# Kernel tuning notes

Hardware: AMD Instinct MI355X
Metric: run time of the kernel (lower is better)

Reference implementation:

```python
import jax, jax.numpy as jnp
import numpy as np

CE_W, TRI_W, CEN_W, ALN_W, BAL_W = 1.0, 1.0, 0.0005, 0.5, 0.1
LS_EPS = 0.1      # label smoothing
MARGIN = 0.3      # triplet margin
F_ALPHA, F_GAMMA = 0.25, 2.0


def setup_inputs() -> dict:
    key = jax.random.key(0)
    ks = jax.random.split(key, 7)
    B, C, D = 1024, 8000, 2048
    return {
        "logits": jax.random.normal(ks[0], (B, C), jnp.float32),
        "features": jax.random.normal(ks[1], (B, D), jnp.float32),
        "feat_rgb": jax.random.normal(ks[2], (B, D), jnp.float32),
        "feat_ir": jax.random.normal(ks[3], (B, D), jnp.float32),
        "modality_weights": jax.random.uniform(ks[4], (B, 2), jnp.float32),
        "centers": jax.random.uniform(ks[5], (C, D), jnp.float32, -1.0, 1.0),
        "labels": jax.random.randint(ks[6], (B,), 0, 64),
    }


def reference(logits, features, feat_rgb, feat_ir, modality_weights, centers, labels):
    B, C = logits.shape
    logp = jax.nn.log_softmax(logits, axis=-1)                      # [B, C]
    logp_y = jnp.take_along_axis(logp, labels[:, None], axis=1)[:, 0]
    # CrossEntropy with label smoothing 0.1 (torch semantics)
    ce = jnp.mean(-(1.0 - LS_EPS) * logp_y - LS_EPS * jnp.mean(logp, axis=-1))
    # Focal loss (faithful to source: uses logpt, so term is <= 0)
    ce_ns = -logp_y
    pt = jnp.exp(-ce_ns)
    focal = jnp.mean(F_ALPHA * (1.0 - pt) ** F_GAMMA * (-ce_ns))
    # Batch-hard triplet (vectorized replacement for per-row python loop)
    sq = jnp.sum(features ** 2, axis=1)
    d2 = jnp.maximum(sq[:, None] + sq[None, :] - 2.0 * (features @ features.T), 0.0)
    dist = jnp.where(d2 > 0, jnp.sqrt(jnp.where(d2 > 0, d2, 1.0)), 0.0)  # safe sqrt
    eq = labels[:, None] == labels[None, :]
    eye = jnp.eye(B, dtype=bool)
    pos_mask = eq & ~eye
    neg_mask = ~eq
    hp = jnp.max(jnp.where(pos_mask, dist, -1.0), axis=1)   # hardest positive
    hn = jnp.min(jnp.where(neg_mask, dist, 1e9), axis=1)    # hardest negative
    valid = jnp.any(pos_mask, axis=1) & jnp.any(neg_mask, axis=1)
    tl = jax.nn.relu(hp - hn + MARGIN)
    triplet = jnp.sum(jnp.where(valid, tl, 0.0)) / jnp.maximum(jnp.sum(valid), 1)
    # Center loss (centers gathered and detached)
    cen = jnp.mean((features - jax.lax.stop_gradient(centers[labels])) ** 2)
    # Modality alignment (single rgb-ir pair): mean(1 - cos)
    f1 = feat_rgb / jnp.maximum(jnp.linalg.norm(feat_rgb, axis=1, keepdims=True), 1e-12)
    f2 = feat_ir / jnp.maximum(jnp.linalg.norm(feat_ir, axis=1, keepdims=True), 1e-12)
    align = jnp.mean(1.0 - jnp.sum(f1 * f2, axis=1))
    # Modality balance: max_entropy - entropy
    ent = jnp.mean(-jnp.sum(modality_weights * jnp.log(modality_weights + 1e-8), axis=1))
    balance = jnp.log(jnp.float32(modality_weights.shape[1])) - ent
    # Modality consistency: mse to detached mean over modalities
    mean_feat = jax.lax.stop_gradient(0.5 * (feat_rgb + feat_ir))
    cons = 0.5 * (jnp.mean((feat_rgb - mean_feat) ** 2) + jnp.mean((feat_ir - mean_feat) ** 2))
    total = (CE_W * (0.7 * ce + 0.3 * focal) + TRI_W * triplet + CEN_W * cen
             + ALN_W * align + BAL_W * balance + 0.1 * cons)
    return jnp.stack([total, ce, focal, triplet, cen, align, balance, cons])
```

## Files before the change

kernel.cpp:

```cpp
#include <hip/hip_runtime.h>
#include <math.h>

#define NB 1024
#define NC 8000
#define ND 2048
#define FBS 2080

#define WS_SQ   0
#define WS_CE   1024
#define WS_FO   2048
#define WS_CEN  3072
#define WS_AL   4096
#define WS_CO   5120
#define WS_HPM  6144
#define WS_HNM  22528
#define WS_FB_BYTES 262144

#define NTILES 136
#define NT     32

typedef __attribute__((ext_vector_type(8))) short bf16x8;
typedef __attribute__((ext_vector_type(4))) float f32x4;
#define GLOB __attribute__((address_space(1)))
#define LDSP __attribute__((address_space(3)))

__device__ inline unsigned short f2bf(float f) {
    unsigned u = __float_as_uint(f);
    u += 0x7FFFu + ((u >> 16) & 1u);
    return (unsigned short)(u >> 16);
}

__global__ __launch_bounds__(256) void k_feat(const float* __restrict__ F,
                                              const float* __restrict__ RGB,
                                              const float* __restrict__ IR,
                                              const float* __restrict__ CEN,
                                              const int* __restrict__ labels,
                                              float* __restrict__ ws,
                                              unsigned short* __restrict__ Fb) {
    const int tid = threadIdx.x;
    const int lane = tid & 63, wid = tid >> 6;
    const int row = blockIdx.x * 4 + wid;
    const float4* f4 = (const float4*)(F + (size_t)row * ND);
    const float4* c4 = (const float4*)(CEN + (size_t)labels[row] * ND);
    const float4* r4 = (const float4*)(RGB + (size_t)row * ND);
    const float4* g4 = (const float4*)(IR + (size_t)row * ND);
    ushort4* fb4 = (ushort4*)(Fb + (size_t)row * FBS);

    float s_ff = 0, s_fc = 0, s_rr = 0, s_ii = 0, s_ri = 0, s_dd = 0;
#pragma unroll 4
    for (int t = 0; t < (ND / 4) / 64; ++t) {
        const int q = t * 64 + lane;
        float4 f = f4[q], c = c4[q], r = r4[q], g = g4[q];
        ushort4 h;
        h.x = f2bf(f.x); h.y = f2bf(f.y); h.z = f2bf(f.z); h.w = f2bf(f.w);
        fb4[q] = h;
        float fa[4] = {f.x, f.y, f.z, f.w};
        float ca[4] = {c.x, c.y, c.z, c.w};
        float ra[4] = {r.x, r.y, r.z, r.w};
        float ga[4] = {g.x, g.y, g.z, g.w};
#pragma unroll
        for (int k = 0; k < 4; ++k) {
            s_ff = fmaf(fa[k], fa[k], s_ff);
            float d = fa[k] - ca[k];
            s_fc = fmaf(d, d, s_fc);
            s_rr = fmaf(ra[k], ra[k], s_rr);
            s_ii = fmaf(ga[k], ga[k], s_ii);
            s_ri = fmaf(ra[k], ga[k], s_ri);
            float e = ra[k] - ga[k];
            s_dd = fmaf(e, e, s_dd);
        }
    }
#pragma unroll
    for (int off = 32; off > 0; off >>= 1) {
        s_ff += __shfl_down(s_ff, off);
        s_fc += __shfl_down(s_fc, off);
        s_rr += __shfl_down(s_rr, off);
        s_ii += __shfl_down(s_ii, off);
        s_ri += __shfl_down(s_ri, off);
        s_dd += __shfl_down(s_dd, off);
    }
    if (lane == 0) {
        ws[WS_SQ + row] = s_ff;
        ws[WS_CEN + row] = s_fc;
        float nr = fmaxf(sqrtf(s_rr), 1e-12f);
        float ni = fmaxf(sqrtf(s_ii), 1e-12f);
        ws[WS_AL + row] = 1.0f - s_ri / (nr * ni);
        ws[WS_CO + row] = s_dd;
    }
}

__global__ __launch_bounds__(256) void k_main(const unsigned short* __restrict__ Fb,
                                              const float* __restrict__ logits,
                                              const int* __restrict__ labels,
                                              float* __restrict__ ws) {
    __shared__ __align__(16) unsigned short As[2][64 * 64];
    __shared__ __align__(16) unsigned short Bs[2][64 * 64];
    __shared__ int lr[64], lc[64];
    __shared__ float sqr[64], sqc[64];
    __shared__ float hplR[64], hnlR[64], hplC[64], hnlC[64];
    __shared__ float rs[4], rsx[4];

    const int tid = threadIdx.x;
    const int lane = tid & 63, wid = tid >> 6;

    if (blockIdx.x < NTILES) {
        int rem = blockIdx.x, rp = 0;
        while (rem >= 16 - rp) { rem -= 16 - rp; rp++; }
        const int cp = rp + rem;
        const int row0 = rp << 6, col0 = cp << 6;
        const float* sq = ws + WS_SQ;

        if (tid < 64) {
            lr[tid] = labels[row0 + tid];
            sqr[tid] = sq[row0 + tid];
            hplR[tid] = -1.0f;
            hnlR[tid] = 1e9f;
        } else if (tid < 128) {
            int t = tid - 64;
            lc[t] = labels[col0 + t];
            sqc[t] = sq[col0 + t];
            hplC[t] = -1.0f;
            hnlC[t] = 1e9f;
        }

        const int r8 = lane >> 3;
        const int sl = lane & 7;
        const int soEl = ((sl ^ r8) * 8);

#define STAGE(IT, BUF) do {                                                              \
    const int k0_ = (IT) * 64;                                                           \
    _Pragma("unroll")                                                                    \
    for (int t = 0; t < 2; ++t) {                                                        \
        const int rb_ = wid * 16 + t * 8;                                                \
        __builtin_amdgcn_global_load_lds(                                                \
            (const GLOB unsigned int*)(Fb + (size_t)(row0 + rb_ + r8) * FBS + k0_ + soEl),\
            (LDSP unsigned int*)&As[BUF][rb_ * 64], 16, 0, 0);                           \
        __builtin_amdgcn_global_load_lds(                                                \
            (const GLOB unsigned int*)(Fb + (size_t)(col0 + rb_ + r8) * FBS + k0_ + soEl),\
            (LDSP unsigned int*)&Bs[BUF][rb_ * 64], 16, 0, 0);                           \
    }                                                                                    \
} while (0)

        const int wr = wid >> 1, wc = wid & 1;
        f32x4 acc[2][2] = {};

        STAGE(0, 0);
        int cur = 0;
#pragma unroll 1
        for (int it = 0; it < NT; ++it) {
            if (it + 1 < NT) {
                STAGE(it + 1, cur ^ 1);
                asm volatile("s_waitcnt vmcnt(4)" ::: "memory");
            } else {
                asm volatile("s_waitcnt vmcnt(0)" ::: "memory");
            }
            __builtin_amdgcn_sched_barrier(0);
            __builtin_amdgcn_s_barrier();

            const char* Ab = (const char*)&As[cur][0];
            const char* Bb = (const char*)&Bs[cur][0];
#pragma unroll
            for (int kk = 0; kk < 2; ++kk) {
                const int kb = kk * 64 + (lane >> 4) * 16;
                const int xo = (lane & 7) << 4;
                bf16x8 a[2], b[2];
#pragma unroll
                for (int mi = 0; mi < 2; ++mi) {
                    const int rt = wr * 32 + mi * 16 + (lane & 15);
                    a[mi] = *(const bf16x8*)(Ab + rt * 128 + (kb ^ xo));
                }
#pragma unroll
                for (int ni = 0; ni < 2; ++ni) {
                    const int ct = wc * 32 + ni * 16 + (lane & 15);
                    b[ni] = *(const bf16x8*)(Bb + ct * 128 + (kb ^ xo));
                }
#pragma unroll
                for (int mi = 0; mi < 2; ++mi)
#pragma unroll
                    for (int ni = 0; ni < 2; ++ni)
                        acc[mi][ni] = __builtin_amdgcn_mfma_f32_16x16x32_bf16(a[mi], b[ni], acc[mi][ni], 0, 0, 0);
            }

            __builtin_amdgcn_sched_barrier(0);
            __builtin_amdgcn_s_barrier();
            cur ^= 1;
        }
#undef STAGE

#pragma unroll
        for (int mi = 0; mi < 2; ++mi) {
#pragma unroll
            for (int reg = 0; reg < 4; ++reg) {
                const int rt = wr * 32 + mi * 16 + (lane >> 4) * 4 + reg;
                const int lbr = lr[rt];
                const float sr = sqr[rt];
                float myhp = -1.0f, myhn = 1e9f;
#pragma unroll
                for (int ni = 0; ni < 2; ++ni) {
                    const int ct = wc * 32 + ni * 16 + (lane & 15);
                    float d2 = sr + sqc[ct] - 2.0f * acc[mi][ni][reg];
                    float dist = sqrtf(fmaxf(d2, 0.0f));
                    if (row0 + rt != col0 + ct) {
                        if (lbr == lc[ct]) myhp = fmaxf(myhp, dist);
                        else               myhn = fminf(myhn, dist);
                    }
                }
#pragma unroll
                for (int off = 1; off < 16; off <<= 1) {
                    myhp = fmaxf(myhp, __shfl_xor(myhp, off, 16));
                    myhn = fminf(myhn, __shfl_xor(myhn, off, 16));
                }
                if ((lane & 15) == 0) {
                    atomicMax((int*)&hplR[rt], __float_as_int(myhp));
                    atomicMin((int*)&hnlR[rt], __float_as_int(myhn));
                }
            }
        }

        if (rp != cp) {
#pragma unroll
            for (int ni = 0; ni < 2; ++ni) {
                const int ct = wc * 32 + ni * 16 + (lane & 15);
                const int lbc = lc[ct];
                const float sc = sqc[ct];
                float myhp = -1.0f, myhn = 1e9f;
#pragma unroll
                for (int mi = 0; mi < 2; ++mi) {
#pragma unroll
                    for (int reg = 0; reg < 4; ++reg) {
                        const int rt = wr * 32 + mi * 16 + (lane >> 4) * 4 + reg;
                        float d2 = sqr[rt] + sc - 2.0f * acc[mi][ni][reg];
                        float dist = sqrtf(fmaxf(d2, 0.0f));
                        if (lr[rt] == lbc) myhp = fmaxf(myhp, dist);
                        else               myhn = fminf(myhn, dist);
                    }
                }
                myhp = fmaxf(myhp, __shfl_xor(myhp, 16));
                myhn = fminf(myhn, __shfl_xor(myhn, 16));
                myhp = fmaxf(myhp, __shfl_xor(myhp, 32));
                myhn = fminf(myhn, __shfl_xor(myhn, 32));
                if ((lane >> 4) == 0) {
                    atomicMax((int*)&hplC[ct], __float_as_int(myhp));
                    atomicMin((int*)&hnlC[ct], __float_as_int(myhn));
                }
            }
        }
        __syncthreads();
        if (tid < 64) {
            ws[WS_HPM + (size_t)(row0 + tid) * 16 + cp] = hplR[tid];
            ws[WS_HNM + (size_t)(row0 + tid) * 16 + cp] = hnlR[tid];
        } else if (tid < 128 && rp != cp) {
            int t = tid - 64;
            ws[WS_HPM + (size_t)(col0 + t) * 16 + rp] = hplC[t];
            ws[WS_HNM + (size_t)(col0 + t) * 16 + rp] = hnlC[t];
        }
    } else {
        const int row = blockIdx.x - NTILES;
        const float* x = logits + (size_t)row * NC;
        const float4* x4 = (const float4*)x;
        float xl = 0.0f;
        if (tid == 0) xl = x[labels[row]];

        float s = 0.0f, sx = 0.0f;
        for (int q = tid; q < NC / 4; q += 256) {
            float4 v = x4[q];
            float vv[4] = {v.x, v.y, v.z, v.w};
#pragma unroll
            for (int c = 0; c < 4; ++c) {
                sx += vv[c];
                s += __expf(vv[c]);
            }
        }
#pragma unroll
        for (int off = 32; off > 0; off >>= 1) {
            s  += __shfl_down(s, off);
            sx += __shfl_down(sx, off);
        }
        if (lane == 0) { rs[wid] = s; rsx[wid] = sx; }
        __syncthreads();
        if (tid == 0) {
            s = rs[0] + rs[1] + rs[2] + rs[3];
            sx = rsx[0] + rsx[1] + rsx[2] + rsx[3];
            const float lse = __logf(s);
            const float logp_y = xl - lse;
            const float mean_logp = sx * (1.0f / NC) - lse;
            const float pt = __expf(logp_y);
            ws[WS_CE + row] = -(1.0f - 0.1f) * logp_y - 0.1f * mean_logp;
            ws[WS_FO + row] = 0.25f * (1.0f - pt) * (1.0f - pt) * logp_y;
        }
    }
}

__global__ __launch_bounds__(256) void k_fin(const float* __restrict__ mw,
                                             float* __restrict__ ws,
                                             float* __restrict__ out) {
    const int tid = threadIdx.x;
    float sum_tl = 0.0f, ent = 0.0f, sce = 0.0f, sfo = 0.0f;
    float scen = 0.0f, sal = 0.0f, sco = 0.0f;
    int cnt = 0;
#pragma unroll
    for (int t = 0; t < 4; ++t) {
        const int i = tid + t * 256;
        const float4* hp4 = (const float4*)(ws + WS_HPM + (size_t)i * 16);
        const float4* hn4 = (const float4*)(ws + WS_HNM + (size_t)i * 16);
        float h1 = -1.0f, h2 = 1e9f;
#pragma unroll
        for (int c = 0; c < 4; ++c) {
            float4 p = hp4[c], n = hn4[c];
            h1 = fmaxf(h1, fmaxf(fmaxf(p.x, p.y), fmaxf(p.z, p.w)));
            h2 = fminf(h2, fminf(fminf(n.x, n.y), fminf(n.z, n.w)));
        }
        if (h1 >= 0.0f && h2 < 1e8f) { sum_tl += fmaxf(h1 - h2 + 0.3f, 0.0f); cnt++; }
        sce += ws[WS_CE + i];
        sfo += ws[WS_FO + i];
        scen += ws[WS_CEN + i];
        sal += ws[WS_AL + i];
        sco += ws[WS_CO + i];
        float w0 = mw[2 * i], w1 = mw[2 * i + 1];
        ent -= w0 * __logf(w0 + 1e-8f) + w1 * __logf(w1 + 1e-8f);
    }
#pragma unroll
    for (int off = 32; off > 0; off >>= 1) {
        sum_tl += __shfl_down(sum_tl, off);
        ent += __shfl_down(ent, off);
        sce += __shfl_down(sce, off);
        sfo += __shfl_down(sfo, off);
        scen += __shfl_down(scen, off);
        sal += __shfl_down(sal, off);
        sco += __shfl_down(sco, off);
        cnt += __shfl_down(cnt, off);
    }
    __shared__ float red[4][7];
    __shared__ int rc[4];
    const int lane = tid & 63, wid = tid >> 6;
    if (lane == 0) {
        red[wid][0] = sum_tl; red[wid][1] = ent; red[wid][2] = sce; red[wid][3] = sfo;
        red[wid][4] = scen; red[wid][5] = sal; red[wid][6] = sco;
        rc[wid] = cnt;
    }
    __syncthreads();
    if (tid == 0) {
#pragma unroll
        for (int w = 1; w < 4; ++w) {
            red[0][0] += red[w][0]; red[0][1] += red[w][1]; red[0][2] += red[w][2];
            red[0][3] += red[w][3]; red[0][4] += red[w][4]; red[0][5] += red[w][5];
            red[0][6] += red[w][6];
            rc[0] += rc[w];
        }
        const float ce = red[0][2] * (1.0f / NB);
        const float focal = red[0][3] * (1.0f / NB);
        const float triplet = red[0][0] / (float)(rc[0] > 0 ? rc[0] : 1);
        const float cen = red[0][4] * (1.0f / ((float)NB * ND));
        const float align = red[0][5] * (1.0f / NB);
        const float balance = logf(2.0f) - red[0][1] * (1.0f / NB);
        const float cons = 0.25f * red[0][6] * (1.0f / ((float)NB * ND));
        const float total = 1.0f * (0.7f * ce + 0.3f * focal) + 1.0f * triplet
                          + 0.0005f * cen + 0.5f * align + 0.1f * balance + 0.1f * cons;
        out[0] = total; out[1] = ce; out[2] = focal; out[3] = triplet;
        out[4] = cen; out[5] = align; out[6] = balance; out[7] = cons;
    }
}

extern "C" void kernel_launch(void* const* d_in, const int* in_sizes, int n_in,
                              void* d_out, int out_size, void* d_ws, size_t ws_size,
                              hipStream_t stream) {
    const float* logits   = (const float*)d_in[0];
    const float* features = (const float*)d_in[1];
    const float* feat_rgb = (const float*)d_in[2];
    const float* feat_ir  = (const float*)d_in[3];
    const float* mw       = (const float*)d_in[4];
    const float* centers  = (const float*)d_in[5];
    const int*   labels   = (const int*)d_in[6];
    float* ws  = (float*)d_ws;
    unsigned short* Fb = (unsigned short*)((char*)d_ws + WS_FB_BYTES);
    float* out = (float*)d_out;

    k_feat<<<dim3(256), dim3(256), 0, stream>>>(features, feat_rgb, feat_ir,
                                                centers, labels, ws, Fb);
    k_main<<<dim3(NTILES + NB), dim3(256), 0, stream>>>(Fb, logits, labels, ws);
    k_fin<<<dim3(1), dim3(256), 0, stream>>>(mw, ws, out);
}
```

Baseline: 43.08 us.

## Move logits reduction into the feature pre-pass and split feature rows per block

The cross-entropy/logsumexp row reduction moves out of the GEMM kernel into the first kernel, which now runs 2048 blocks: one per feature row and one per logits row. Feature rows are handled by a whole 256-thread block instead of one wave, with a shared-memory cross-wave reduction. The distance kernel then launches only the 136 GEMM tiles. This is meant to run the bandwidth-bound work with more parallelism and overlap it earlier, so the small GEMM grid is not tail-bound behind logits blocks. The cost is that the GEMM no longer overlaps with the logits streaming.

```diff
diff --git a/kernel.cpp b/kernel.cpp
--- a/kernel.cpp
+++ b/kernel.cpp
@@ -30,67 +30,116 @@
     return (unsigned short)(u >> 16);
 }
 
-__global__ __launch_bounds__(256) void k_feat(const float* __restrict__ F,
-                                              const float* __restrict__ RGB,
-                                              const float* __restrict__ IR,
-                                              const float* __restrict__ CEN,
-                                              const int* __restrict__ labels,
-                                              float* __restrict__ ws,
-                                              unsigned short* __restrict__ Fb) {
+__global__ __launch_bounds__(256) void k_pre(const float* __restrict__ logits,
+                                             const float* __restrict__ F,
+                                             const float* __restrict__ RGB,
+                                             const float* __restrict__ IR,
+                                             const float* __restrict__ CEN,
+                                             const int* __restrict__ labels,
+                                             float* __restrict__ ws,
+                                             unsigned short* __restrict__ Fb) {
+    __shared__ float red[4][6];
+    __shared__ float rs[4], rsx[4];
     const int tid = threadIdx.x;
     const int lane = tid & 63, wid = tid >> 6;
-    const int row = blockIdx.x * 4 + wid;
-    const float4* f4 = (const float4*)(F + (size_t)row * ND);
-    const float4* c4 = (const float4*)(CEN + (size_t)labels[row] * ND);
-    const float4* r4 = (const float4*)(RGB + (size_t)row * ND);
-    const float4* g4 = (const float4*)(IR + (size_t)row * ND);
-    ushort4* fb4 = (ushort4*)(Fb + (size_t)row * FBS);
-
-    float s_ff = 0, s_fc = 0, s_rr = 0, s_ii = 0, s_ri = 0, s_dd = 0;
-#pragma unroll 4
-    for (int t = 0; t < (ND / 4) / 64; ++t) {
-        const int q = t * 64 + lane;
-        float4 f = f4[q], c = c4[q], r = r4[q], g = g4[q];
-        ushort4 h;
-        h.x = f2bf(f.x); h.y = f2bf(f.y); h.z = f2bf(f.z); h.w = f2bf(f.w);
-        fb4[q] = h;
-        float fa[4] = {f.x, f.y, f.z, f.w};
-        float ca[4] = {c.x, c.y, c.z, c.w};
-        float ra[4] = {r.x, r.y, r.z, r.w};
-        float ga[4] = {g.x, g.y, g.z, g.w};
-#pragma unroll
-        for (int k = 0; k < 4; ++k) {
-            s_ff = fmaf(fa[k], fa[k], s_ff);
-            float d = fa[k] - ca[k];
-            s_fc = fmaf(d, d, s_fc);
-            s_rr = fmaf(ra[k], ra[k], s_rr);
-            s_ii = fmaf(ga[k], ga[k], s_ii);
-            s_ri = fmaf(ra[k], ga[k], s_ri);
-            float e = ra[k] - ga[k];
-            s_dd = fmaf(e, e, s_dd);
-        }
-    }
-#pragma unroll
-    for (int off = 32; off > 0; off >>= 1) {
-        s_ff += __shfl_down(s_ff, off);
-        s_fc += __shfl_down(s_fc, off);
-        s_rr += __shfl_down(s_rr, off);
-        s_ii += __shfl_down(s_ii, off);
-        s_ri += __shfl_down(s_ri, off);
-        s_dd += __shfl_down(s_dd, off);
-    }
-    if (lane == 0) {
-        ws[WS_SQ + row] = s_ff;
-        ws[WS_CEN + row] = s_fc;
-        float nr = fmaxf(sqrtf(s_rr), 1e-12f);
-        float ni = fmaxf(sqrtf(s_ii), 1e-12f);
-        ws[WS_AL + row] = 1.0f - s_ri / (nr * ni);
-        ws[WS_CO + row] = s_dd;
-    }
-}
-
-__global__ __launch_bounds__(256) void k_main(const unsigned short* __restrict__ Fb,
-                                              const float* __restrict__ logits,
+
+    if (blockIdx.x < NB) {
+        const int row = blockIdx.x;
+        const float4* f4 = (const float4*)(F + (size_t)row * ND);
+        const float4* c4 = (const float4*)(CEN + (size_t)labels[row] * ND);
+        const float4* r4 = (const float4*)(RGB + (size_t)row * ND);
+        const float4* g4 = (const float4*)(IR + (size_t)row * ND);
+        ushort4* fb4 = (ushort4*)(Fb + (size_t)row * FBS);
+
+        float s_ff = 0, s_fc = 0, s_rr = 0, s_ii = 0, s_ri = 0, s_dd = 0;
+#pragma unroll
+        for (int t = 0; t < 2; ++t) {
+            const int q = tid + t * 256;
+            float4 f = f4[q], c = c4[q], r = r4[q], g = g4[q];
+            ushort4 h;
+            h.x = f2bf(f.x); h.y = f2bf(f.y); h.z = f2bf(f.z); h.w = f2bf(f.w);
+            fb4[q] = h;
+            float fa[4] = {f.x, f.y, f.z, f.w};
+            float ca[4] = {c.x, c.y, c.z, c.w};
+            float ra[4] = {r.x, r.y, r.z, r.w};
+            float ga[4] = {g.x, g.y, g.z, g.w};
+#pragma unroll
+            for (int k = 0; k < 4; ++k) {
+                s_ff = fmaf(fa[k], fa[k], s_ff);
+                float d = fa[k] - ca[k];
+                s_fc = fmaf(d, d, s_fc);
+                s_rr = fmaf(ra[k], ra[k], s_rr);
+                s_ii = fmaf(ga[k], ga[k], s_ii);
+                s_ri = fmaf(ra[k], ga[k], s_ri);
+                float e = ra[k] - ga[k];
+                s_dd = fmaf(e, e, s_dd);
+            }
+        }
+#pragma unroll
+        for (int off = 32; off > 0; off >>= 1) {
+            s_ff += __shfl_down(s_ff, off);
+            s_fc += __shfl_down(s_fc, off);
+            s_rr += __shfl_down(s_rr, off);
+            s_ii += __shfl_down(s_ii, off);
+            s_ri += __shfl_down(s_ri, off);
+            s_dd += __shfl_down(s_dd, off);
+        }
+        if (lane == 0) {
+            red[wid][0] = s_ff; red[wid][1] = s_fc; red[wid][2] = s_rr;
+            red[wid][3] = s_ii; red[wid][4] = s_ri; red[wid][5] = s_dd;
+        }
+        __syncthreads();
+        if (tid == 0) {
+#pragma unroll
+            for (int w = 1; w < 4; ++w) {
+                red[0][0] += red[w][0]; red[0][1] += red[w][1]; red[0][2] += red[w][2];
+                red[0][3] += red[w][3]; red[0][4] += red[w][4]; red[0][5] += red[w][5];
+            }
+            ws[WS_SQ + row] = red[0][0];
+            ws[WS_CEN + row] = red[0][1];
+            float nr = fmaxf(sqrtf(red[0][2]), 1e-12f);
+            float ni = fmaxf(sqrtf(red[0][3]), 1e-12f);
+            ws[WS_AL + row] = 1.0f - red[0][4] / (nr * ni);
+            ws[WS_CO + row] = red[0][5];
+        }
+    } else {
+        const int row = blockIdx.x - NB;
+        const float* x = logits + (size_t)row * NC;
+        const float4* x4 = (const float4*)x;
+        float xl = 0.0f;
+        if (tid == 0) xl = x[labels[row]];
+
+        float s = 0.0f, sx = 0.0f;
+        for (int q = tid; q < NC / 4; q += 256) {
+            float4 v = x4[q];
+            float vv[4] = {v.x, v.y, v.z, v.w};
+#pragma unroll
+            for (int c = 0; c < 4; ++c) {
+                sx += vv[c];
+                s += __expf(vv[c]);
+            }
+        }
+#pragma unroll
+        for (int off = 32; off > 0; off >>= 1) {
+            s  += __shfl_down(s, off);
+            sx += __shfl_down(sx, off);
+        }
+        if (lane == 0) { rs[wid] = s; rsx[wid] = sx; }
+        __syncthreads();
+        if (tid == 0) {
+            s = rs[0] + rs[1] + rs[2] + rs[3];
+            sx = rsx[0] + rsx[1] + rsx[2] + rsx[3];
+            const float lse = __logf(s);
+            const float logp_y = xl - lse;
+            const float mean_logp = sx * (1.0f / NC) - lse;
+            const float pt = __expf(logp_y);
+            ws[WS_CE + row] = -(1.0f - 0.1f) * logp_y - 0.1f * mean_logp;
+            ws[WS_FO + row] = 0.25f * (1.0f - pt) * (1.0f - pt) * logp_y;
+        }
+    }
+}
+
+__global__ __launch_bounds__(256) void k_dist(const unsigned short* __restrict__ Fb,
                                               const int* __restrict__ labels,
                                               float* __restrict__ ws) {
     __shared__ __align__(16) unsigned short As[2][64 * 64];
@@ -98,34 +147,32 @@
     __shared__ int lr[64], lc[64];
     __shared__ float sqr[64], sqc[64];
     __shared__ float hplR[64], hnlR[64], hplC[64], hnlC[64];
-    __shared__ float rs[4], rsx[4];
 
     const int tid = threadIdx.x;
     const int lane = tid & 63, wid = tid >> 6;
 
-    if (blockIdx.x < NTILES) {
-        int rem = blockIdx.x, rp = 0;
-        while (rem >= 16 - rp) { rem -= 16 - rp; rp++; }
-        const int cp = rp + rem;
-        const int row0 = rp << 6, col0 = cp << 6;
-        const float* sq = ws + WS_SQ;
-
-        if (tid < 64) {
-            lr[tid] = labels[row0 + tid];
-            sqr[tid] = sq[row0 + tid];
-            hplR[tid] = -1.0f;
-            hnlR[tid] = 1e9f;
-        } else if (tid < 128) {
-            int t = tid - 64;
-            lc[t] = labels[col0 + t];
-            sqc[t] = sq[col0 + t];
-            hplC[t] = -1.0f;
-            hnlC[t] = 1e9f;
-        }
-
-        const int r8 = lane >> 3;
-        const int sl = lane & 7;
-        const int soEl = ((sl ^ r8) * 8);
+    int rem = blockIdx.x, rp = 0;
+    while (rem >= 16 - rp) { rem -= 16 - rp; rp++; }
+    const int cp = rp + rem;
+    const int row0 = rp << 6, col0 = cp << 6;
+    const float* sq = ws + WS_SQ;
+
+    if (tid < 64) {
+        lr[tid] = labels[row0 + tid];
+        sqr[tid] = sq[row0 + tid];
+        hplR[tid] = -1.0f;
+        hnlR[tid] = 1e9f;
+    } else if (tid < 128) {
+        int t = tid - 64;
+        lc[t] = labels[col0 + t];
+        sqc[t] = sq[col0 + t];
+        hplC[t] = -1.0f;
+        hnlC[t] = 1e9f;
+    }
+
+    const int r8 = lane >> 3;
+    const int sl = lane & 7;
+    const int soEl = ((sl ^ r8) * 8);
 
 #define STAGE(IT, BUF) do {                                                              \
     const int k0_ = (IT) * 64;                                                           \
@@ -141,153 +188,118 @@
     }                                                                                    \
 } while (0)
 
-        const int wr = wid >> 1, wc = wid & 1;
-        f32x4 acc[2][2] = {};
-
-        STAGE(0, 0);
-        int cur = 0;
+    const int wr = wid >> 1, wc = wid & 1;
+    f32x4 acc[2][2] = {};
+
+    STAGE(0, 0);
+    int cur = 0;
 #pragma unroll 1
-        for (int it = 0; it < NT; ++it) {
-            if (it + 1 < NT) {
-                STAGE(it + 1, cur ^ 1);
-                asm volatile("s_waitcnt vmcnt(4)" ::: "memory");
-            } else {
-                asm volatile("s_waitcnt vmcnt(0)" ::: "memory");
-            }
-            __builtin_amdgcn_sched_barrier(0);
-            __builtin_amdgcn_s_barrier();
-
-            const char* Ab = (const char*)&As[cur][0];
-            const char* Bb = (const char*)&Bs[cur][0];
-#pragma unroll
-            for (int kk = 0; kk < 2; ++kk) {
-                const int kb = kk * 64 + (lane >> 4) * 16;
-                const int xo = (lane & 7) << 4;
-                bf16x8 a[2], b[2];
-#pragma unroll
-                for (int mi = 0; mi < 2; ++mi) {
-                    const int rt = wr * 32 + mi * 16 + (lane & 15);
-                    a[mi] = *(const bf16x8*)(Ab + rt * 128 + (kb ^ xo));
-                }
-#pragma unroll
-                for (int ni = 0; ni < 2; ++ni) {
-                    const int ct = wc * 32 + ni * 16 + (lane & 15);
-                    b[ni] = *(const bf16x8*)(Bb + ct * 128 + (kb ^ xo));
-                }
-#pragma unroll
-                for (int mi = 0; mi < 2; ++mi)
-#pragma unroll
-                    for (int ni = 0; ni < 2; ++ni)
-                        acc[mi][ni] = __builtin_amdgcn_mfma_f32_16x16x32_bf16(a[mi], b[ni], acc[mi][ni], 0, 0, 0);
-            }
-
-            __builtin_amdgcn_sched_barrier(0);
-            __builtin_amdgcn_s_barrier();
-            cur ^= 1;
-        }
-#undef STAGE
-
-#pragma unroll
-        for (int mi = 0; mi < 2; ++mi) {
-#pragma unroll
-            for (int reg = 0; reg < 4; ++reg) {
-                const int rt = wr * 32 + mi * 16 + (lane >> 4) * 4 + reg;
-                const int lbr = lr[rt];
-                const float sr = sqr[rt];
-                float myhp = -1.0f, myhn = 1e9f;
-#pragma unroll
-                for (int ni = 0; ni < 2; ++ni) {
-                    const int ct = wc * 32 + ni * 16 + (lane & 15);
-                    float d2 = sr + sqc[ct] - 2.0f * acc[mi][ni][reg];
-                    float dist = sqrtf(fmaxf(d2, 0.0f));
-                    if (row0 + rt != col0 + ct) {
-                        if (lbr == lc[ct]) myhp = fmaxf(myhp, dist);
-                        else               myhn = fminf(myhn, dist);
-                    }
-                }
-#pragma unroll
-                for (int off = 1; off < 16; off <<= 1) {
-                    myhp = fmaxf(myhp, __shfl_xor(myhp, off, 16));
-                    myhn = fminf(myhn, __shfl_xor(myhn, off, 16));
-                }
-                if ((lane & 15) == 0) {
-                    atomicMax((int*)&hplR[rt], __float_as_int(myhp));
-                    atomicMin((int*)&hnlR[rt], __float_as_int(myhn));
-                }
-            }
-        }
-
-        if (rp != cp) {
+    for (int it = 0; it < NT; ++it) {
+        if (it + 1 < NT) {
+            STAGE(it + 1, cur ^ 1);
+            asm volatile("s_waitcnt vmcnt(4)" ::: "memory");
+        } else {
+            asm volatile("s_waitcnt vmcnt(0)" ::: "memory");
+        }
+        __builtin_amdgcn_sched_barrier(0);
+        __builtin_amdgcn_s_barrier();
+
+        const char* Ab = (const char*)&As[cur][0];
+        const char* Bb = (const char*)&Bs[cur][0];
+#pragma unroll
+        for (int kk = 0; kk < 2; ++kk) {
+            const int kb = kk * 64 + (lane >> 4) * 16;
+            const int xo = (lane & 7) << 4;
+            bf16x8 a[2], b[2];
+#pragma unroll
+            for (int mi = 0; mi < 2; ++mi) {
+                const int rt = wr * 32 + mi * 16 + (lane & 15);
+                a[mi] = *(const bf16x8*)(Ab + rt * 128 + (kb ^ xo));
+            }
 #pragma unroll
             for (int ni = 0; ni < 2; ++ni) {
                 const int ct = wc * 32 + ni * 16 + (lane & 15);
-                const int lbc = lc[ct];
-                const float sc = sqc[ct];
-                float myhp = -1.0f, myhn = 1e9f;
-#pragma unroll
-                for (int mi = 0; mi < 2; ++mi) {
-#pragma unroll
-                    for (int reg = 0; reg < 4; ++reg) {
-                        const int rt = wr * 32 + mi * 16 + (lane >> 4) * 4 + reg;
-                        float d2 = sqr[rt] + sc - 2.0f * acc[mi][ni][reg];
-                        float dist = sqrtf(fmaxf(d2, 0.0f));
-                        if (lr[rt] == lbc) myhp = fmaxf(myhp, dist);
-                        else               myhn = fminf(myhn, dist);
-                    }
+                b[ni] = *(const bf16x8*)(Bb + ct * 128 + (kb ^ xo));
+            }
+#pragma unroll
+            for (int mi = 0; mi < 2; ++mi)
+#pragma unroll
+                for (int ni = 0; ni < 2; ++ni)
+                    acc[mi][ni] = __builtin_amdgcn_mfma_f32_16x16x32_bf16(a[mi], b[ni], acc[mi][ni], 0, 0, 0);
+        }
+
+        __builtin_amdgcn_sched_barrier(0);
+        __builtin_amdgcn_s_barrier();
+        cur ^= 1;
+    }
+#undef STAGE
+
+#pragma unroll
+    for (int mi = 0; mi < 2; ++mi) {
+#pragma unroll
+        for (int reg = 0; reg < 4; ++reg) {
+            const int rt = wr * 32 + mi * 16 + (lane >> 4) * 4 + reg;
+            const int lbr = lr[rt];
+            const float sr = sqr[rt];
+            float myhp = -1.0f, myhn = 1e9f;
+#pragma unroll
+            for (int ni = 0; ni < 2; ++ni) {
+                const int ct = wc * 32 + ni * 16 + (lane & 15);
+                float d2 = sr + sqc[ct] - 2.0f * acc[mi][ni][reg];
+                float dist = sqrtf(fmaxf(d2, 0.0f));
+                if (row0 + rt != col0 + ct) {
+                    if (lbr == lc[ct]) myhp = fmaxf(myhp, dist);
+                    else               myhn = fminf(myhn, dist);
                 }
-                myhp = fmaxf(myhp, __shfl_xor(myhp, 16));
-                myhn = fminf(myhn, __shfl_xor(myhn, 16));
-                myhp = fmaxf(myhp, __shfl_xor(myhp, 32));
-                myhn = fminf(myhn, __shfl_xor(myhn, 32));
-                if ((lane >> 4) == 0) {
-                    atomicMax((int*)&hplC[ct], __float_as_int(myhp));
-                    atomicMin((int*)&hnlC[ct], __float_as_int(myhn));
+            }
+#pragma unroll
+            for (int off = 1; off < 16; off <<= 1) {
+                myhp = fmaxf(myhp, __shfl_xor(myhp, off, 16));
+                myhn = fminf(myhn, __shfl_xor(myhn, off, 16));
+            }
+            if ((lane & 15) == 0) {
+                atomicMax((int*)&hplR[rt], __float_as_int(myhp));
+                atomicMin((int*)&hnlR[rt], __float_as_int(myhn));
+            }
+        }
+    }
+
+    if (rp != cp) {
+#pragma unroll
+        for (int ni = 0; ni < 2; ++ni) {
+            const int ct = wc * 32 + ni * 16 + (lane & 15);
+            const int lbc = lc[ct];
+            const float sc = sqc[ct];
+            float myhp = -1.0f, myhn = 1e9f;
+#pragma unroll
+            for (int mi = 0; mi < 2; ++mi) {
+#pragma unroll
+                for (int reg = 0; reg < 4; ++reg) {
+                    const int rt = wr * 32 + mi * 16 + (lane >> 4) * 4 + reg;
+                    float d2 = sqr[rt] + sc - 2.0f * acc[mi][ni][reg];
+                    float dist = sqrtf(fmaxf(d2, 0.0f));
+                    if (lr[rt] == lbc) myhp = fmaxf(myhp, dist);
+                    else               myhn = fminf(myhn, dist);
                 }
             }
-        }
-        __syncthreads();
-        if (tid < 64) {
-            ws[WS_HPM + (size_t)(row0 + tid) * 16 + cp] = hplR[tid];
-            ws[WS_HNM + (size_t)(row0 + tid) * 16 + cp] = hnlR[tid];
-        } else if (tid < 128 && rp != cp) {
-            int t = tid - 64;
-            ws[WS_HPM + (size_t)(col0 + t) * 16 + rp] = hplC[t];
-            ws[WS_HNM + (size_t)(col0 + t) * 16 + rp] = hnlC[t];
-        }
-    } else {
-        const int row = blockIdx.x - NTILES;
-        const float* x = logits + (size_t)row * NC;
-        const float4* x4 = (const float4*)x;
-        float xl = 0.0f;
-        if (tid == 0) xl = x[labels[row]];
-
-        float s = 0.0f, sx = 0.0f;
-        for (int q = tid; q < NC / 4; q += 256) {
-            float4 v = x4[q];
-            float vv[4] = {v.x, v.y, v.z, v.w};
-#pragma unroll
-            for (int c = 0; c < 4; ++c) {
-                sx += vv[c];
-                s += __expf(vv[c]);
-            }
-        }
-#pragma unroll
-        for (int off = 32; off > 0; off >>= 1) {
-            s  += __shfl_down(s, off);
-            sx += __shfl_down(sx, off);
-        }
-        if (lane == 0) { rs[wid] = s; rsx[wid] = sx; }
-        __syncthreads();
-        if (tid == 0) {
-            s = rs[0] + rs[1] + rs[2] + rs[3];
-            sx = rsx[0] + rsx[1] + rsx[2] + rsx[3];
-            const float lse = __logf(s);
-            const float logp_y = xl - lse;
-            const float mean_logp = sx * (1.0f / NC) - lse;
-            const float pt = __expf(logp_y);
-            ws[WS_CE + row] = -(1.0f - 0.1f) * logp_y - 0.1f * mean_logp;
-            ws[WS_FO + row] = 0.25f * (1.0f - pt) * (1.0f - pt) * logp_y;
-        }
+            myhp = fmaxf(myhp, __shfl_xor(myhp, 16));
+            myhn = fminf(myhn, __shfl_xor(myhn, 16));
+            myhp = fmaxf(myhp, __shfl_xor(myhp, 32));
+            myhn = fminf(myhn, __shfl_xor(myhn, 32));
+            if ((lane >> 4) == 0) {
+                atomicMax((int*)&hplC[ct], __float_as_int(myhp));
+                atomicMin((int*)&hnlC[ct], __float_as_int(myhn));
+            }
+        }
+    }
+    __syncthreads();
+    if (tid < 64) {
+        ws[WS_HPM + (size_t)(row0 + tid) * 16 + cp] = hplR[tid];
+        ws[WS_HNM + (size_t)(row0 + tid) * 16 + cp] = hnlR[tid];
+    } else if (tid < 128 && rp != cp) {
+        int t = tid - 64;
+        ws[WS_HPM + (size_t)(col0 + t) * 16 + rp] = hplC[t];
+        ws[WS_HNM + (size_t)(col0 + t) * 16 + rp] = hnlC[t];
     }
 }
 
@@ -375,8 +387,8 @@
     unsigned short* Fb = (unsigned short*)((char*)d_ws + WS_FB_BYTES);
     float* out = (float*)d_out;
 
-    k_feat<<<dim3(256), dim3(256), 0, stream>>>(features, feat_rgb, feat_ir,
-                                                centers, labels, ws, Fb);
-    k_main<<<dim3(NTILES + NB), dim3(256), 0, stream>>>(Fb, logits, labels, ws);
+    k_pre<<<dim3(2 * NB), dim3(256), 0, stream>>>(logits, features, feat_rgb, feat_ir,
+                                                  centers, labels, ws, Fb);
+    k_dist<<<dim3(NTILES), dim3(256), 0, stream>>>(Fb, labels, ws);
     k_fin<<<dim3(1), dim3(256), 0, stream>>>(mw, ws, out);
 }
```

New measurement: 44.67 us. +3.7%, slower.
